# Kernel optimization log

Hardware: AMD Instinct MI355X
Metric: run time of the kernel (lower is better)

The kernel has to match this reference:

```python
import jax, jax.numpy as jnp
import numpy as np

N = 262144          # number of coordinate points
IN = 3              # coordinate dim
FF = 256            # fourier feature dim (out_features)
NFREQ = FF // 2     # 128 frequencies
H = 256             # mlp hidden width
L = 4               # hidden sine layers
OUT = 2             # Fullmodel hard-codes out_features=2 for the MLP
OMEGA0 = 30.0


def setup_inputs() -> dict:
    key = jax.random.key(0)
    ks = jax.random.split(key, 12)
    x = jax.random.normal(ks[0], (N, IN), dtype=jnp.float32)
    # Fourier encoder params (non-trainable in torch, still float inputs here)
    scales = jnp.ones((1, IN), dtype=jnp.float32)  # coordinate_scales = [1,1,1]
    B = jax.random.normal(ks[1], (IN, NFREQ), dtype=jnp.float32) * 3.0 * 10.0  # N(0,3)*10
    # SIREN first layer: uniform(-1/in, 1/in), in = FF
    W0 = jax.random.uniform(ks[2], (H, FF), dtype=jnp.float32, minval=-1.0 / FF, maxval=1.0 / FF)
    b0 = jax.random.uniform(ks[3], (H,), dtype=jnp.float32, minval=-1.0 / np.sqrt(FF), maxval=1.0 / np.sqrt(FF))
    # Hidden sine layers: uniform(-sqrt(6/in), sqrt(6/in)), in = H
    c = float(np.sqrt(6.0 / H))
    Wh = jax.random.uniform(ks[4], (L, H, H), dtype=jnp.float32, minval=-c, maxval=c)
    bh = jax.random.uniform(ks[5], (L, H), dtype=jnp.float32, minval=-1.0 / np.sqrt(H), maxval=1.0 / np.sqrt(H))
    # Final plain linear H -> OUT (default torch init, any small values fine)
    Wf = jax.random.uniform(ks[6], (OUT, H), dtype=jnp.float32, minval=-1.0 / np.sqrt(H), maxval=1.0 / np.sqrt(H))
    bf = jax.random.uniform(ks[7], (OUT,), dtype=jnp.float32, minval=-1.0 / np.sqrt(H), maxval=1.0 / np.sqrt(H))
    return {"x": x, "scales": scales, "B": B, "W0": W0, "b0": b0,
            "Wh": Wh, "bh": bh, "Wf": Wf, "bf": bf}


def reference(x, scales, B, W0, b0, Wh, bh, Wf, bf):
    # Fourier feature map: sqrt(2) * [sin(proj), cos(proj)]
    proj = (x * scales) @ B                                   # [N, NFREQ]
    sqrt2 = jnp.float32(np.sqrt(2.0))
    h = jnp.concatenate([jnp.sin(proj), jnp.cos(proj)], axis=-1) * sqrt2  # [N, FF]
    # First SIREN layer: sin(omega0 * (W x + b))
    h = jnp.sin(OMEGA0 * (h @ W0.T + b0))                     # [N, H]
    # Hidden sine layers: sin(W x + b)
    for i in range(L):
        h = jnp.sin(h @ Wh[i].T + bh[i])                      # [N, H]
    return h @ Wf.T + bf                                      # [N, OUT]
```

## Files before the change

### kernel.cpp

```cpp
#include <hip/hip_runtime.h>
#include <hip/hip_bf16.h>


typedef __attribute__((ext_vector_type(8))) short bf16x8;
typedef __attribute__((ext_vector_type(4))) float f32x4;

#define NTOTAL 262144
#define BM 64
#define HD 256
#define INV2PI 0.15915494309189535f

__device__ __forceinline__ unsigned short f2bf(float f) {
    unsigned int u = __float_as_uint(f);
    u += 0x7FFFu + ((u >> 16) & 1u);
    return (unsigned short)(u >> 16);
}

__device__ __forceinline__ unsigned int pk2(float a, float b) {
    __hip_bfloat162 h = __float22bfloat162_rn(make_float2(a, b));
    union { __hip_bfloat162 h; unsigned int u; } c;
    c.h = h;
    return c.u;
}

__device__ __forceinline__ float sin_rev(float rev) {
    return __builtin_amdgcn_sinf(__builtin_amdgcn_fractf(rev));
}

__device__ __forceinline__ int a_off(int r, int byte) {
    return r * 512 + (byte ^ ((r & 7) << 4));
}

__global__ void convert_w(const float* __restrict__ W0, const float* __restrict__ Wh,
                          const float* __restrict__ Wf, unsigned short* __restrict__ wb) {
    const int i = blockIdx.x * 256 + threadIdx.x;
    if (i < 327680) {
        const int l = i >> 16, rem = i & 65535;
        const int j = rem >> 8, k = rem & 255;
        const float v = (l == 0) ? W0[rem] * 1.41421356237309515f : Wh[i - 65536];
        const int jt = j >> 4, kt = k >> 5, q = (k >> 3) & 3, r = j & 15, t = k & 7;
        const int dst = (l << 16) + (((jt << 3) + kt) << 9) + (((q << 4) + r) << 3) + t;
        wb[dst] = f2bf(v);
    }
    if (i < 4096)
        wb[327680 + i] = (i < 512) ? f2bf(Wf[i]) : (unsigned short)0;
}

__global__ __launch_bounds__(256, 4) void siren_fused(
    const float* __restrict__ x, const float* __restrict__ scales,
    const float* __restrict__ Bm, const float* __restrict__ b0,
    const float* __restrict__ bh, const float* __restrict__ bfin,
    const unsigned short* __restrict__ wb, float* __restrict__ out) {

    __shared__ __align__(16) unsigned short A[BM * HD];

    const int tid  = threadIdx.x;
    const int lane = tid & 63;
    const int wid  = tid >> 6;
    const int row0 = blockIdx.x * BM;
    const int arow = lane & 15;
    const int q    = lane >> 4;
    const int kq   = q * 8;

    {
        const int r  = tid >> 2;
        const int c0 = (tid & 3) * 32;
        const float* xr = x + (row0 + r) * 3;
        const float x0 = xr[0] * scales[0] * INV2PI;
        const float x1 = xr[1] * scales[1] * INV2PI;
        const float x2 = xr[2] * scales[2] * INV2PI;
        #pragma unroll
        for (int cc = 0; cc < 32; cc += 8) {
            const int c = c0 + cc;
            float sv[8], cv[8];
            #pragma unroll
            for (int t = 0; t < 8; ++t) {
                const float rev = x0 * Bm[c + t] + x1 * Bm[128 + c + t] + x2 * Bm[256 + c + t];
                const float fr  = __builtin_amdgcn_fractf(rev);
                sv[t] = __builtin_amdgcn_sinf(fr);
                cv[t] = __builtin_amdgcn_cosf(fr);
            }
            uint4 us, uc;
            us.x = pk2(sv[0], sv[1]); us.y = pk2(sv[2], sv[3]);
            us.z = pk2(sv[4], sv[5]); us.w = pk2(sv[6], sv[7]);
            uc.x = pk2(cv[0], cv[1]); uc.y = pk2(cv[2], cv[3]);
            uc.z = pk2(cv[4], cv[5]); uc.w = pk2(cv[6], cv[7]);
            *(uint4*)((char*)A + a_off(r, 2 * c))         = us;
            *(uint4*)((char*)A + a_off(r, 2 * (c + 128))) = uc;
        }
    }

    #pragma unroll 1
    for (int layer = 0; layer < 5; ++layer) {
        const unsigned short* Wl = wb + (layer << 16);

        __syncthreads();

        f32x4 acc[4][4];
        #pragma unroll
        for (int a = 0; a < 4; ++a)
            #pragma unroll
            for (int b = 0; b < 4; ++b)
                acc[a][b] = (f32x4)(0.0f);

        #pragma unroll
        for (int kt = 0; kt < 8; ++kt) {
            bf16x8 wf[4], hf[4];
            #pragma unroll
            for (int jt = 0; jt < 4; ++jt)
                wf[jt] = *(const bf16x8*)(Wl +
                    ((((wid * 4 + jt) << 3) + kt) << 9) + lane * 8);
            #pragma unroll
            for (int rt = 0; rt < 4; ++rt)
                hf[rt] = *(const bf16x8*)((const char*)A +
                    a_off(rt * 16 + arow, kt * 64 + q * 16));
            #pragma unroll
            for (int jt = 0; jt < 4; ++jt)
                #pragma unroll
                for (int rt = 0; rt < 4; ++rt)
                    acc[jt][rt] = __builtin_amdgcn_mfma_f32_16x16x32_bf16(
                        wf[jt], hf[rt], acc[jt][rt], 0, 0, 0);
        }

        __syncthreads();

        const float s = (layer == 0) ? (30.0f * INV2PI) : INV2PI;
        const float* bias = (layer == 0) ? b0 : (bh + (layer - 1) * HD);
        #pragma unroll
        for (int jt = 0; jt < 4; ++jt) {
            const int jj = wid * 64 + jt * 16 + q * 4;
            float4 bv = *(const float4*)(bias + jj);
            bv.x *= s; bv.y *= s; bv.z *= s; bv.w *= s;
            #pragma unroll
            for (int rt = 0; rt < 4; ++rt) {
                const int r = rt * 16 + arow;
                const float s0 = sin_rev(fmaf(acc[jt][rt][0], s, bv.x));
                const float s1 = sin_rev(fmaf(acc[jt][rt][1], s, bv.y));
                const float s2 = sin_rev(fmaf(acc[jt][rt][2], s, bv.z));
                const float s3 = sin_rev(fmaf(acc[jt][rt][3], s, bv.w));
                uint2 val;
                val.x = pk2(s0, s1);
                val.y = pk2(s2, s3);
                *(uint2*)((char*)A + a_off(r, jj * 2)) = val;
            }
        }
    }

    __syncthreads();

    {
        const unsigned short* Wfp = wb + 327680;
        f32x4 acc = (f32x4)(0.0f);
        #pragma unroll
        for (int kt = 0; kt < 8; ++kt) {
            const bf16x8 ff = *(const bf16x8*)(Wfp + arow * HD + kt * 32 + kq);
            const bf16x8 hf = *(const bf16x8*)((const char*)A +
                a_off(wid * 16 + arow, kt * 64 + q * 16));
            acc = __builtin_amdgcn_mfma_f32_16x16x32_bf16(ff, hf, acc, 0, 0, 0);
        }
        if (q == 0) {
            const int rg = row0 + wid * 16 + arow;
            float2 o;
            o.x = acc[0] + bfin[0];
            o.y = acc[1] + bfin[1];
            *(float2*)(out + rg * 2) = o;
        }
    }
}

extern "C" void kernel_launch(void* const* d_in, const int* in_sizes, int n_in,
                              void* d_out, int out_size, void* d_ws, size_t ws_size,
                              hipStream_t stream) {
    (void)in_sizes; (void)n_in; (void)out_size; (void)ws_size;
    const float* x      = (const float*)d_in[0];
    const float* scales = (const float*)d_in[1];
    const float* Bm     = (const float*)d_in[2];
    const float* W0     = (const float*)d_in[3];
    const float* b0     = (const float*)d_in[4];
    const float* Wh     = (const float*)d_in[5];
    const float* bh     = (const float*)d_in[6];
    const float* Wf     = (const float*)d_in[7];
    const float* bf     = (const float*)d_in[8];
    unsigned short* wb  = (unsigned short*)d_ws;

    hipLaunchKernelGGL(convert_w, dim3(1280), dim3(256), 0, stream, W0, Wh, Wf, wb);
    hipLaunchKernelGGL(siren_fused, dim3(NTOTAL / BM), dim3(256), 0, stream,
                       x, scales, Bm, b0, bh, bf, wb, (float*)d_out);
}
```

Before: 228.5 us.

## Interleave per-column-tile sine epilogue with MFMA loop and double-buffer fragment loads

The per-layer GEMM is restructured from one accumulator set of 4x4 tiles into a sequential loop over output column tiles, each with 4 accumulators. The bias+sine epilogue for each column tile runs right after its MFMAs, and the packed results are held in registers until after the barrier. Weight and activation fragments are double-buffered one step ahead, the LDS swizzle widens from 8 to 16 rows, and launch bounds drop to 3 blocks per CU. The aim is to overlap transcendental work with matrix ops and cut accumulator pressure, at the cost of reloading the A fragments from LDS four times per layer and possibly lower occupancy.

Result: no change. 228.9 us (+0.2%).

```diff
diff --git a/kernel.cpp b/kernel.cpp
--- a/kernel.cpp
+++ b/kernel.cpp
@@ -28,7 +28,7 @@
 }
 
 __device__ __forceinline__ int a_off(int r, int byte) {
-    return r * 512 + (byte ^ ((r & 7) << 4));
+    return r * 512 + (byte ^ ((r & 15) << 4));
 }
 
 __global__ void convert_w(const float* __restrict__ W0, const float* __restrict__ Wh,
@@ -46,7 +46,7 @@
         wb[327680 + i] = (i < 512) ? f2bf(Wf[i]) : (unsigned short)0;
 }
 
-__global__ __launch_bounds__(256, 4) void siren_fused(
+__global__ __launch_bounds__(256, 3) void siren_fused(
     const float* __restrict__ x, const float* __restrict__ scales,
     const float* __restrict__ Bm, const float* __restrict__ b0,
     const float* __restrict__ bh, const float* __restrict__ bfin,
@@ -93,56 +93,66 @@
     #pragma unroll 1
     for (int layer = 0; layer < 5; ++layer) {
         const unsigned short* Wl = wb + (layer << 16);
+        const float s = (layer == 0) ? (30.0f * INV2PI) : INV2PI;
+        const float* bias = (layer == 0) ? b0 : (bh + (layer - 1) * HD);
 
         __syncthreads();
 
-        f32x4 acc[4][4];
+        uint2 hold[4][4];
+        f32x4 acc[4];
+        bf16x8 wfbuf[2], hfbuf[2][4];
+
+        wfbuf[0] = *(const bf16x8*)(Wl + (((wid * 4) << 3) << 9) + lane * 8);
         #pragma unroll
-        for (int a = 0; a < 4; ++a)
-            #pragma unroll
-            for (int b = 0; b < 4; ++b)
-                acc[a][b] = (f32x4)(0.0f);
+        for (int rt = 0; rt < 4; ++rt)
+            hfbuf[0][rt] = *(const bf16x8*)((const char*)A +
+                a_off(rt * 16 + arow, q * 16));
 
         #pragma unroll
-        for (int kt = 0; kt < 8; ++kt) {
-            bf16x8 wf[4], hf[4];
-            #pragma unroll
-            for (int jt = 0; jt < 4; ++jt)
-                wf[jt] = *(const bf16x8*)(Wl +
-                    ((((wid * 4 + jt) << 3) + kt) << 9) + lane * 8);
+        for (int u = 0; u < 32; ++u) {
+            const int jt = u >> 3, kt = u & 7;
+            const int cur = u & 1, nxt = cur ^ 1;
+            if (kt == 0) {
+                #pragma unroll
+                for (int rt = 0; rt < 4; ++rt) acc[rt] = (f32x4)(0.0f);
+            }
+            if (u < 31) {
+                const int jt1 = (u + 1) >> 3, kt1 = (u + 1) & 7;
+                wfbuf[nxt] = *(const bf16x8*)(Wl +
+                    ((((wid * 4 + jt1) << 3) + kt1) << 9) + lane * 8);
+                #pragma unroll
+                for (int rt = 0; rt < 4; ++rt)
+                    hfbuf[nxt][rt] = *(const bf16x8*)((const char*)A +
+                        a_off(rt * 16 + arow, kt1 * 64 + q * 16));
+            }
             #pragma unroll
             for (int rt = 0; rt < 4; ++rt)
-                hf[rt] = *(const bf16x8*)((const char*)A +
-                    a_off(rt * 16 + arow, kt * 64 + q * 16));
-            #pragma unroll
-            for (int jt = 0; jt < 4; ++jt)
+                acc[rt] = __builtin_amdgcn_mfma_f32_16x16x32_bf16(
+                    wfbuf[cur], hfbuf[cur][rt], acc[rt], 0, 0, 0);
+            if (kt == 7) {
+                const int jj = wid * 64 + jt * 16 + q * 4;
+                float4 bv = *(const float4*)(bias + jj);
+                bv.x *= s; bv.y *= s; bv.z *= s; bv.w *= s;
                 #pragma unroll
-                for (int rt = 0; rt < 4; ++rt)
-                    acc[jt][rt] = __builtin_amdgcn_mfma_f32_16x16x32_bf16(
-                        wf[jt], hf[rt], acc[jt][rt], 0, 0, 0);
+                for (int rt = 0; rt < 4; ++rt) {
+                    const float s0 = sin_rev(fmaf(acc[rt][0], s, bv.x));
+                    const float s1 = sin_rev(fmaf(acc[rt][1], s, bv.y));
+                    const float s2 = sin_rev(fmaf(acc[rt][2], s, bv.z));
+                    const float s3 = sin_rev(fmaf(acc[rt][3], s, bv.w));
+                    hold[jt][rt].x = pk2(s0, s1);
+                    hold[jt][rt].y = pk2(s2, s3);
+                }
+            }
         }
 
         __syncthreads();
 
-        const float s = (layer == 0) ? (30.0f * INV2PI) : INV2PI;
-        const float* bias = (layer == 0) ? b0 : (bh + (layer - 1) * HD);
         #pragma unroll
         for (int jt = 0; jt < 4; ++jt) {
             const int jj = wid * 64 + jt * 16 + q * 4;
-            float4 bv = *(const float4*)(bias + jj);
-            bv.x *= s; bv.y *= s; bv.z *= s; bv.w *= s;
             #pragma unroll
-            for (int rt = 0; rt < 4; ++rt) {
-                const int r = rt * 16 + arow;
-                const float s0 = sin_rev(fmaf(acc[jt][rt][0], s, bv.x));
-                const float s1 = sin_rev(fmaf(acc[jt][rt][1], s, bv.y));
-                const float s2 = sin_rev(fmaf(acc[jt][rt][2], s, bv.z));
-                const float s3 = sin_rev(fmaf(acc[jt][rt][3], s, bv.w));
-                uint2 val;
-                val.x = pk2(s0, s1);
-                val.y = pk2(s2, s3);
-                *(uint2*)((char*)A + a_off(r, jj * 2)) = val;
-            }
+            for (int rt = 0; rt < 4; ++rt)
+                *(uint2*)((char*)A + a_off(rt * 16 + arow, jj * 2)) = hold[jt][rt];
         }
     }
 
```
